# Performance work log

Measured on AMD Instinct MI355X. Metric: run time of the kernel, lower is better.

## Reference

```python
import jax, jax.numpy as jnp
import numpy as np

B, L, DM, H, PD = 2, 1024, 512, 8, 64
D = DM // H  # head_dim = 64
NEG = -10000.0


def setup_inputs() -> dict:
    key = jax.random.key(0)
    ks = jax.random.split(key, 12)
    s = 1.0 / np.sqrt(DM)
    sp = 1.0 / np.sqrt(PD)
    return {
        "x": jax.random.normal(ks[0], (B, L, DM), dtype=jnp.float32),
        "z": jax.random.normal(ks[1], (B, L, L, PD), dtype=jnp.float32),
        "residue_mask": jnp.ones((B, L), dtype=bool),
        "Wq": jax.random.normal(ks[2], (DM, DM), dtype=jnp.float32) * s,
        "bq": jnp.zeros((DM,), dtype=jnp.float32),
        "Wk": jax.random.normal(ks[3], (DM, DM), dtype=jnp.float32) * s,
        "bk": jnp.zeros((DM,), dtype=jnp.float32),
        "Wv": jax.random.normal(ks[4], (DM, DM), dtype=jnp.float32) * s,
        "bv": jnp.zeros((DM,), dtype=jnp.float32),
        "Wo": jax.random.normal(ks[5], (DM, DM), dtype=jnp.float32) * s,
        "bo": jnp.zeros((DM,), dtype=jnp.float32),
        "Wpb": jax.random.normal(ks[6], (PD, H), dtype=jnp.float32) * sp,
    }


def reference(x, z, residue_mask, Wq, bq, Wk, bk, Wv, bv, Wo, bo, Wpb):
    b, l, c = x.shape
    scale = 1.0 / np.sqrt(D)
    # projections -> (B, H, L, D)
    q = (x @ Wq + bq).reshape(b, l, H, D).transpose(0, 2, 1, 3)
    k = (x @ Wk + bk).reshape(b, l, H, D).transpose(0, 2, 1, 3)
    v = (x @ Wv + bv).reshape(b, l, H, D).transpose(0, 2, 1, 3)
    # pair bias: (B, L, L, PD) @ (PD, H) -> (B, H, L, L)
    bias = jnp.einsum('bijp,ph->bhij', z, Wpb)
    logits = jnp.einsum('bhid,bhjd->bhij', q, k) * scale + bias
    key_ok = residue_mask[:, None, None, :]
    query_ok = residue_mask[:, None, :, None]
    logits = jnp.where(key_ok, logits, NEG)
    logits = jnp.where(query_ok, logits, NEG)
    attn = jax.nn.softmax(logits, axis=-1)
    out = jnp.einsum('bhij,bhjd->bhid', attn, v)
    out = out.transpose(0, 2, 1, 3).reshape(b, l, c)
    return out @ Wo + bo
```

## Files before the change

### kernel.cpp

```cpp
#include <hip/hip_runtime.h>

typedef __bf16 bf16;
typedef __attribute__((ext_vector_type(4))) __bf16 bf16x4;
typedef __attribute__((ext_vector_type(8))) __bf16 bf16x8;
typedef __attribute__((ext_vector_type(4))) float f32x4;
typedef __attribute__((ext_vector_type(4))) _Float16 f16x4;
typedef __attribute__((ext_vector_type(2))) _Float16 f16x2;

#define B_   2
#define L_   1024
#define DM_  512
#define H_   8
#define D_   64
#define PD_  64
#define NEG_VAL -10000.0f

#define XB_N   (2048*512)
#define WT_N   (1536*512)
#define WTO_N  (512*512)
#define WTPB_N (16*64)

static __device__ __forceinline__ f32x4 mfma_bf16(bf16x8 a, bf16x8 b, f32x4 c) {
  return __builtin_amdgcn_mfma_f32_16x16x32_bf16(a, b, c, 0, 0, 0);
}

__global__ __launch_bounds__(256) void prep_kernel(
    const float* __restrict__ x, const float* __restrict__ Wq, const float* __restrict__ Wk,
    const float* __restrict__ Wv, const float* __restrict__ Wo, const float* __restrict__ Wpb,
    bf16* __restrict__ xb, bf16* __restrict__ Wt, bf16* __restrict__ Wto, bf16* __restrict__ Wtpb) {
  const int total = XB_N + WT_N + WTO_N + WTPB_N;
  for (int idx = blockIdx.x * 256 + threadIdx.x; idx < total; idx += gridDim.x * 256) {
    if (idx < XB_N) {
      xb[idx] = (bf16)x[idx];
    } else if (idx < XB_N + WT_N) {
      int t = idx - XB_N;
      int n = t >> 9, kk = t & 511;
      int sel = n >> 9, nn = n & 511;
      const float* W = sel == 0 ? Wq : (sel == 1 ? Wk : Wv);
      Wt[t] = (bf16)W[kk * 512 + nn];
    } else if (idx < XB_N + WT_N + WTO_N) {
      int t = idx - XB_N - WT_N;
      int n = t >> 9, kk = t & 511;
      Wto[t] = (bf16)Wo[kk * 512 + n];
    } else {
      int t = idx - XB_N - WT_N - WTO_N;
      int n = t >> 6, kk = t & 63;
      Wtpb[t] = (n < 8) ? (bf16)Wpb[kk * 8 + n] : (bf16)0.0f;
    }
  }
}

__global__ __launch_bounds__(256) void qkv_gemm(
    const bf16* __restrict__ xb, const bf16* __restrict__ Wt,
    const float* __restrict__ bq, const float* __restrict__ bk, const float* __restrict__ bv,
    bf16* __restrict__ qb, bf16* __restrict__ kb, bf16* __restrict__ vT) {
  int wid = blockIdx.x * 4 + (threadIdx.x >> 6);
  int lane = threadIdx.x & 63;
  int mt = wid / 48, nt = wid - mt * 48;
  int row0 = mt * 32, col0 = nt * 32;
  int lr = lane & 15, lg = lane >> 4;
  const bf16* a0p = xb + (row0 + lr) * 512 + lg * 8;
  const bf16* a1p = a0p + 16 * 512;
  const bf16* b0p = Wt + (col0 + lr) * 512 + lg * 8;
  const bf16* b1p = b0p + 16 * 512;
  f32x4 acc00 = {0.f,0.f,0.f,0.f}, acc01 = acc00, acc10 = acc00, acc11 = acc00;
#pragma unroll
  for (int kk = 0; kk < 512; kk += 32) {
    bf16x8 a0 = *reinterpret_cast<const bf16x8*>(a0p + kk);
    bf16x8 a1 = *reinterpret_cast<const bf16x8*>(a1p + kk);
    bf16x8 b0 = *reinterpret_cast<const bf16x8*>(b0p + kk);
    bf16x8 b1 = *reinterpret_cast<const bf16x8*>(b1p + kk);
    acc00 = mfma_bf16(a0, b0, acc00);
    acc01 = mfma_bf16(a0, b1, acc01);
    acc10 = mfma_bf16(a1, b0, acc10);
    acc11 = mfma_bf16(a1, b1, acc11);
  }
#pragma unroll
  for (int ni = 0; ni < 2; ++ni) {
    int col = col0 + ni * 16 + lr;
    int wsel = col >> 9;
    int ncol = col & 511;
    int h = ncol >> 6, d = ncol & 63;
    const float* bias = wsel == 0 ? bq : (wsel == 1 ? bk : bv);
    float bval = bias[ncol];
#pragma unroll
    for (int mi = 0; mi < 2; ++mi) {
      f32x4 acc = (mi == 0) ? (ni == 0 ? acc00 : acc01) : (ni == 0 ? acc10 : acc11);
      int m0 = row0 + mi * 16 + lg * 4;
      int bidx = m0 >> 10, l0 = m0 & 1023;
      if (wsel == 2) {
        bf16x4 pv;
#pragma unroll
        for (int r = 0; r < 4; ++r) pv[r] = (bf16)(acc[r] + bval);
        *reinterpret_cast<bf16x4*>(vT + ((long)(bidx * H_ + h) * D_ + d) * L_ + l0) = pv;
      } else if (wsel == 0) {
#pragma unroll
        for (int r = 0; r < 4; ++r)
          qb[((long)(bidx * H_ + h) * L_ + l0 + r) * D_ + d] = (bf16)((acc[r] + bval) * 0.125f);
      } else {
#pragma unroll
        for (int r = 0; r < 4; ++r)
          kb[((long)(bidx * H_ + h) * L_ + l0 + r) * D_ + d] = (bf16)(acc[r] + bval);
      }
    }
  }
}

__global__ __launch_bounds__(256) void fused_attn(
    const float* __restrict__ z, const bf16* __restrict__ qb, const bf16* __restrict__ kb,
    const bf16* __restrict__ vT, const bf16* __restrict__ Wtpb, const int* __restrict__ mask,
    _Float16* __restrict__ part_o, float* __restrict__ part_m, float* __restrict__ part_l) {
  __shared__ _Float16 bias_lds[8 * 16 * 64];
  __shared__ bf16 p_lds[4][16 * 64];
  int bid = blockIdx.x;
  int jc = bid & 15, it = (bid >> 4) & 63, b = bid >> 10;
  int i0 = it * 16, j0 = jc * 64;
  int tid = threadIdx.x, w = tid >> 6, lane = tid & 63, lr = lane & 15, lg = lane >> 4;

  bf16x8 wb0 = *reinterpret_cast<const bf16x8*>(Wtpb + lr * 64 + lg * 8);
  bf16x8 wb1 = *reinterpret_cast<const bf16x8*>(Wtpb + lr * 64 + 32 + lg * 8);

  {
    char* bl = (char*)bias_lds;
#pragma unroll
    for (int ii = 0; ii < 4; ++ii) {
      int i = w * 4 + ii;
      const float* zb_ = z + ((long)(b * L_ + i0 + i) * L_ + j0) * 64;
#pragma unroll
      for (int js = 0; js < 4; ++js) {
        const float* zr = zb_ + (js * 16 + lr) * 64 + lg * 8;
        f32x4 f0 = *reinterpret_cast<const f32x4*>(zr);
        f32x4 f1 = *reinterpret_cast<const f32x4*>(zr + 4);
        f32x4 f2 = *reinterpret_cast<const f32x4*>(zr + 32);
        f32x4 f3 = *reinterpret_cast<const f32x4*>(zr + 36);
        bf16x8 a0, a1;
#pragma unroll
        for (int e = 0; e < 4; ++e) {
          a0[e] = (bf16)f0[e]; a0[e + 4] = (bf16)f1[e];
          a1[e] = (bf16)f2[e]; a1[e + 4] = (bf16)f3[e];
        }
        f32x4 c = {0.f, 0.f, 0.f, 0.f};
        c = mfma_bf16(a0, wb0, c);
        c = mfma_bf16(a1, wb1, c);
        if (lr < 8) {
          f16x4 hv;
#pragma unroll
          for (int r = 0; r < 4; ++r) hv[r] = (_Float16)c[r];
          int X = (js * 32 + lg * 8) ^ ((i & 7) << 4) ^ ((lr & 3) << 5);
          *reinterpret_cast<f16x4*>(bl + lr * 2048 + i * 128 + X) = hv;
        }
      }
    }
  }
  __syncthreads();

  bool qok = mask[b * L_ + i0 + lr] != 0;
  char* pbuf = (char*)&p_lds[w][0];
  int swz = (lr & 7) << 4;
  const char* bl = (const char*)bias_lds;

#pragma unroll
  for (int hh = 0; hh < 2; ++hh) {
    int h = w * 2 + hh;
    const bf16* qrow = qb + ((long)(b * H_ + h) * L_ + i0 + lr) * D_ + lg * 8;
    bf16x8 qa0 = *reinterpret_cast<const bf16x8*>(qrow);
    bf16x8 qa1 = *reinterpret_cast<const bf16x8*>(qrow + 32);
    const bf16* kbase = kb + (long)(b * H_ + h) * L_ * D_;
    const bf16* vbase = vT + (long)(b * H_ + h) * D_ * L_;

    f32x4 s0, s1, s2, s3;
#pragma unroll
    for (int tile = 0; tile < 4; ++tile) {
      int X = (tile * 32 + lg * 8) ^ ((lr & 7) << 4) ^ ((h & 3) << 5);
      f16x4 bv = *reinterpret_cast<const f16x4*>(bl + h * 2048 + lr * 128 + X);
      f32x4 acc;
#pragma unroll
      for (int r = 0; r < 4; ++r) acc[r] = (float)bv[r];
      const bf16* kr = kbase + (long)(j0 + tile * 16 + lr) * D_ + lg * 8;
      acc = mfma_bf16(*reinterpret_cast<const bf16x8*>(kr), qa0, acc);
      acc = mfma_bf16(*reinterpret_cast<const bf16x8*>(kr + 32), qa1, acc);
      int4 mk = *reinterpret_cast<const int4*>(mask + b * L_ + j0 + tile * 16 + lg * 4);
      if (mk.x == 0) acc[0] = NEG_VAL;
      if (mk.y == 0) acc[1] = NEG_VAL;
      if (mk.z == 0) acc[2] = NEG_VAL;
      if (mk.w == 0) acc[3] = NEG_VAL;
      if (tile == 0) s0 = acc; else if (tile == 1) s1 = acc; else if (tile == 2) s2 = acc; else s3 = acc;
    }
    if (!qok) {
#pragma unroll
      for (int r = 0; r < 4; ++r) { s0[r] = NEG_VAL; s1[r] = NEG_VAL; s2[r] = NEG_VAL; s3[r] = NEG_VAL; }
    }
    float m = s0[0];
#pragma unroll
    for (int r = 0; r < 4; ++r) m = fmaxf(fmaxf(fmaxf(m, s0[r]), fmaxf(s1[r], s2[r])), s3[r]);
    m = fmaxf(m, __shfl_xor(m, 16));
    m = fmaxf(m, __shfl_xor(m, 32));
    f32x4 p0, p1, p2, p3;
    float ps = 0.f;
#pragma unroll
    for (int r = 0; r < 4; ++r) {
      p0[r] = __expf(s0[r] - m); p1[r] = __expf(s1[r] - m);
      p2[r] = __expf(s2[r] - m); p3[r] = __expf(s3[r] - m);
      ps += p0[r] + p1[r] + p2[r] + p3[r];
    }
    ps += __shfl_xor(ps, 16);
    ps += __shfl_xor(ps, 32);
#pragma unroll
    for (int tile = 0; tile < 4; ++tile) {
      f32x4 pv = (tile == 0) ? p0 : (tile == 1) ? p1 : (tile == 2) ? p2 : p3;
      bf16x4 pb_;
#pragma unroll
      for (int r = 0; r < 4; ++r) pb_[r] = (bf16)pv[r];
      *reinterpret_cast<bf16x4*>(pbuf + ((lr * 128 + tile * 32 + lg * 8) ^ swz)) = pb_;
    }
    bf16x8 pa0 = *reinterpret_cast<const bf16x8*>(pbuf + ((lr * 128 + lg * 16) ^ swz));
    bf16x8 pa1 = *reinterpret_cast<const bf16x8*>(pbuf + ((lr * 128 + 64 + lg * 16) ^ swz));
    long obase = ((long)bid * H_ + h) * 16;
#pragma unroll
    for (int dtile = 0; dtile < 4; ++dtile) {
      const bf16* vr = vbase + (long)(dtile * 16 + lr) * L_ + j0 + lg * 8;
      f32x4 acc = {0.f, 0.f, 0.f, 0.f};
      acc = mfma_bf16(*reinterpret_cast<const bf16x8*>(vr), pa0, acc);
      acc = mfma_bf16(*reinterpret_cast<const bf16x8*>(vr + 32), pa1, acc);
      f16x4 ov;
#pragma unroll
      for (int r = 0; r < 4; ++r) ov[r] = (_Float16)acc[r];
      *reinterpret_cast<f16x4*>(part_o + (obase + lr) * 64 + dtile * 16 + lg * 4) = ov;
    }
    if (lg == 0) { part_m[obase + lr] = m; part_l[obase + lr] = ps; }
  }
}

__global__ __launch_bounds__(256) void merge16(
    const _Float16* __restrict__ part_o, const float* __restrict__ part_m,
    const float* __restrict__ part_l, bf16* __restrict__ attn_out) {
  int t = blockIdx.x * 256 + threadIdx.x;
  int d0 = (t & 15) * 4;
  int row = t >> 4;
  int b = row >> 13, h = (row >> 10) & 7, i = row & 1023;
  int it = i >> 4, il = i & 15;
  int bid0 = (b << 10) + (it << 4);
  float mv[16];
  float M = -3.0e38f;
#pragma unroll
  for (int p = 0; p < 16; ++p) {
    long base = ((long)(bid0 + p) * H_ + h) * 16 + il;
    mv[p] = part_m[base];
    M = fmaxf(M, mv[p]);
  }
  float lt = 0.f;
  float oa[4] = {0.f, 0.f, 0.f, 0.f};
#pragma unroll
  for (int p = 0; p < 16; ++p) {
    long base = ((long)(bid0 + p) * H_ + h) * 16 + il;
    float c = __expf(mv[p] - M);
    lt += c * part_l[base];
    f16x4 ov = *reinterpret_cast<const f16x4*>(part_o + base * 64 + d0);
#pragma unroll
    for (int e = 0; e < 4; ++e) oa[e] += c * (float)ov[e];
  }
  float inv = 1.0f / lt;
  bf16x4 r_;
#pragma unroll
  for (int e = 0; e < 4; ++e) r_[e] = (bf16)(oa[e] * inv);
  *reinterpret_cast<bf16x4*>(attn_out + ((long)(b * L_ + i)) * DM_ + h * D_ + d0) = r_;
}

__global__ __launch_bounds__(256) void out_gemm(
    const bf16* __restrict__ ab, const bf16* __restrict__ Wto,
    const float* __restrict__ bo, float* __restrict__ out) {
  int wid = blockIdx.x * 4 + (threadIdx.x >> 6);
  int lane = threadIdx.x & 63;
  int mt = wid >> 4, nt = wid & 15;
  int row0 = mt * 32, col0 = nt * 32;
  int lr = lane & 15, lg = lane >> 4;
  const bf16* a0p = ab + (row0 + lr) * 512 + lg * 8;
  const bf16* a1p = a0p + 16 * 512;
  const bf16* b0p = Wto + (col0 + lr) * 512 + lg * 8;
  const bf16* b1p = b0p + 16 * 512;
  f32x4 acc00 = {0.f,0.f,0.f,0.f}, acc01 = acc00, acc10 = acc00, acc11 = acc00;
#pragma unroll
  for (int kk = 0; kk < 512; kk += 32) {
    bf16x8 a0 = *reinterpret_cast<const bf16x8*>(a0p + kk);
    bf16x8 a1 = *reinterpret_cast<const bf16x8*>(a1p + kk);
    bf16x8 b0 = *reinterpret_cast<const bf16x8*>(b0p + kk);
    bf16x8 b1 = *reinterpret_cast<const bf16x8*>(b1p + kk);
    acc00 = mfma_bf16(a0, b0, acc00);
    acc01 = mfma_bf16(a0, b1, acc01);
    acc10 = mfma_bf16(a1, b0, acc10);
    acc11 = mfma_bf16(a1, b1, acc11);
  }
#pragma unroll
  for (int ni = 0; ni < 2; ++ni) {
    int col = col0 + ni * 16 + lr;
    float bval = bo[col];
#pragma unroll
    for (int mi = 0; mi < 2; ++mi) {
      f32x4 acc = (mi == 0) ? (ni == 0 ? acc00 : acc01) : (ni == 0 ? acc10 : acc11);
      int m0 = row0 + mi * 16 + lg * 4;
#pragma unroll
      for (int r = 0; r < 4; ++r) out[(long)(m0 + r) * 512 + col] = acc[r] + bval;
    }
  }
}

extern "C" void kernel_launch(void* const* d_in, const int* in_sizes, int n_in,
                              void* d_out, int out_size, void* d_ws, size_t ws_size,
                              hipStream_t stream) {
  const float* x    = (const float*)d_in[0];
  const float* z    = (const float*)d_in[1];
  const int*   mask = (const int*)d_in[2];
  const float* Wq   = (const float*)d_in[3];
  const float* bq   = (const float*)d_in[4];
  const float* Wk   = (const float*)d_in[5];
  const float* bk   = (const float*)d_in[6];
  const float* Wv   = (const float*)d_in[7];
  const float* bv   = (const float*)d_in[8];
  const float* Wo   = (const float*)d_in[9];
  const float* bo   = (const float*)d_in[10];
  const float* Wpb  = (const float*)d_in[11];

  char* ws = (char*)d_ws;
  bf16* xb        = (bf16*)(ws + 0);
  bf16* Wt        = (bf16*)(ws + 2097152);
  bf16* Wto       = (bf16*)(ws + 3670016);
  bf16* Wtpb      = (bf16*)(ws + 4194304);
  bf16* qbuf      = (bf16*)(ws + 4196352);
  bf16* kbuf      = (bf16*)(ws + 6293504);
  bf16* vTbuf     = (bf16*)(ws + 8390656);
  bf16* attn_out  = (bf16*)(ws + 10487808);
  _Float16* part_o = (_Float16*)(ws + 12584960);
  float* part_m   = (float*)(ws + 46139392);
  float* part_l   = (float*)(ws + 47187968);

  prep_kernel<<<2048, 256, 0, stream>>>(x, Wq, Wk, Wv, Wo, Wpb, xb, Wt, Wto, Wtpb);
  qkv_gemm<<<768, 256, 0, stream>>>(xb, Wt, bq, bk, bv, qbuf, kbuf, vTbuf);
  fused_attn<<<2048, 256, 0, stream>>>(z, qbuf, kbuf, vTbuf, Wtpb, mask, part_o, part_m, part_l);
  merge16<<<1024, 256, 0, stream>>>(part_o, part_m, part_l, attn_out);
  out_gemm<<<256, 256, 0, stream>>>(attn_out, Wto, bo, (float*)d_out);
}
```

Measured before the change: 188.5 us.

## Warp-specialize fused attention with double-buffered pair-bias producer warps

```diff
diff --git a/kernel.cpp b/kernel.cpp
--- a/kernel.cpp
+++ b/kernel.cpp
@@ -106,128 +106,176 @@
   }
 }
 
-__global__ __launch_bounds__(256) void fused_attn(
+__global__ __launch_bounds__(512) void fused_attn(
     const float* __restrict__ z, const bf16* __restrict__ qb, const bf16* __restrict__ kb,
     const bf16* __restrict__ vT, const bf16* __restrict__ Wtpb, const int* __restrict__ mask,
     _Float16* __restrict__ part_o, float* __restrict__ part_m, float* __restrict__ part_l) {
-  __shared__ _Float16 bias_lds[8 * 16 * 64];
+  __shared__ _Float16 bias_lds[2][8 * 16 * 64];
   __shared__ bf16 p_lds[4][16 * 64];
   int bid = blockIdx.x;
-  int jc = bid & 15, it = (bid >> 4) & 63, b = bid >> 10;
-  int i0 = it * 16, j0 = jc * 64;
+  int jg = bid & 3, it = (bid >> 2) & 63, b = bid >> 8;
+  int i0 = it * 16;
   int tid = threadIdx.x, w = tid >> 6, lane = tid & 63, lr = lane & 15, lg = lane >> 4;
-
-  bf16x8 wb0 = *reinterpret_cast<const bf16x8*>(Wtpb + lr * 64 + lg * 8);
-  bf16x8 wb1 = *reinterpret_cast<const bf16x8*>(Wtpb + lr * 64 + 32 + lg * 8);
-
-  {
-    char* bl = (char*)bias_lds;
-#pragma unroll
-    for (int ii = 0; ii < 4; ++ii) {
-      int i = w * 4 + ii;
-      const float* zb_ = z + ((long)(b * L_ + i0 + i) * L_ + j0) * 64;
-#pragma unroll
-      for (int js = 0; js < 4; ++js) {
-        const float* zr = zb_ + (js * 16 + lr) * 64 + lg * 8;
-        f32x4 f0 = *reinterpret_cast<const f32x4*>(zr);
-        f32x4 f1 = *reinterpret_cast<const f32x4*>(zr + 4);
-        f32x4 f2 = *reinterpret_cast<const f32x4*>(zr + 32);
-        f32x4 f3 = *reinterpret_cast<const f32x4*>(zr + 36);
-        bf16x8 a0, a1;
-#pragma unroll
-        for (int e = 0; e < 4; ++e) {
-          a0[e] = (bf16)f0[e]; a0[e + 4] = (bf16)f1[e];
-          a1[e] = (bf16)f2[e]; a1[e + 4] = (bf16)f3[e];
-        }
-        f32x4 c = {0.f, 0.f, 0.f, 0.f};
-        c = mfma_bf16(a0, wb0, c);
-        c = mfma_bf16(a1, wb1, c);
-        if (lr < 8) {
-          f16x4 hv;
-#pragma unroll
-          for (int r = 0; r < 4; ++r) hv[r] = (_Float16)c[r];
-          int X = (js * 32 + lg * 8) ^ ((i & 7) << 4) ^ ((lr & 3) << 5);
-          *reinterpret_cast<f16x4*>(bl + lr * 2048 + i * 128 + X) = hv;
+  bool producer = w < 4;
+
+  if (producer) {
+    int pw = w;
+    bf16x8 wb0 = *reinterpret_cast<const bf16x8*>(Wtpb + lr * 64 + lg * 8);
+    bf16x8 wb1 = *reinterpret_cast<const bf16x8*>(Wtpb + lr * 64 + 32 + lg * 8);
+    {
+      char* bl = (char*)&bias_lds[0][0];
+      int j0 = jg * 256;
+#pragma unroll
+      for (int ii = 0; ii < 4; ++ii) {
+        int i = pw * 4 + ii;
+        const float* zb_ = z + ((long)(b * L_ + i0 + i) * L_ + j0) * 64;
+#pragma unroll
+        for (int js = 0; js < 4; ++js) {
+          const float* zr = zb_ + (js * 16 + lr) * 64 + lg * 8;
+          f32x4 f0 = *reinterpret_cast<const f32x4*>(zr);
+          f32x4 f1 = *reinterpret_cast<const f32x4*>(zr + 4);
+          f32x4 f2 = *reinterpret_cast<const f32x4*>(zr + 32);
+          f32x4 f3 = *reinterpret_cast<const f32x4*>(zr + 36);
+          bf16x8 a0, a1;
+#pragma unroll
+          for (int e = 0; e < 4; ++e) {
+            a0[e] = (bf16)f0[e]; a0[e + 4] = (bf16)f1[e];
+            a1[e] = (bf16)f2[e]; a1[e + 4] = (bf16)f3[e];
+          }
+          f32x4 c = {0.f, 0.f, 0.f, 0.f};
+          c = mfma_bf16(a0, wb0, c);
+          c = mfma_bf16(a1, wb1, c);
+          if (lr < 8) {
+            f16x4 hv;
+#pragma unroll
+            for (int r = 0; r < 4; ++r) hv[r] = (_Float16)c[r];
+            int X = (js * 32 + lg * 8) ^ ((i & 7) << 4) ^ ((lr & 3) << 5);
+            *reinterpret_cast<f16x4*>(bl + lr * 2048 + i * 128 + X) = hv;
+          }
         }
       }
     }
-  }
-  __syncthreads();
-
-  bool qok = mask[b * L_ + i0 + lr] != 0;
-  char* pbuf = (char*)&p_lds[w][0];
-  int swz = (lr & 7) << 4;
-  const char* bl = (const char*)bias_lds;
-
-#pragma unroll
-  for (int hh = 0; hh < 2; ++hh) {
-    int h = w * 2 + hh;
-    const bf16* qrow = qb + ((long)(b * H_ + h) * L_ + i0 + lr) * D_ + lg * 8;
-    bf16x8 qa0 = *reinterpret_cast<const bf16x8*>(qrow);
-    bf16x8 qa1 = *reinterpret_cast<const bf16x8*>(qrow + 32);
-    const bf16* kbase = kb + (long)(b * H_ + h) * L_ * D_;
-    const bf16* vbase = vT + (long)(b * H_ + h) * D_ * L_;
-
-    f32x4 s0, s1, s2, s3;
-#pragma unroll
-    for (int tile = 0; tile < 4; ++tile) {
-      int X = (tile * 32 + lg * 8) ^ ((lr & 7) << 4) ^ ((h & 3) << 5);
-      f16x4 bv = *reinterpret_cast<const f16x4*>(bl + h * 2048 + lr * 128 + X);
-      f32x4 acc;
-#pragma unroll
-      for (int r = 0; r < 4; ++r) acc[r] = (float)bv[r];
-      const bf16* kr = kbase + (long)(j0 + tile * 16 + lr) * D_ + lg * 8;
-      acc = mfma_bf16(*reinterpret_cast<const bf16x8*>(kr), qa0, acc);
-      acc = mfma_bf16(*reinterpret_cast<const bf16x8*>(kr + 32), qa1, acc);
-      int4 mk = *reinterpret_cast<const int4*>(mask + b * L_ + j0 + tile * 16 + lg * 4);
-      if (mk.x == 0) acc[0] = NEG_VAL;
-      if (mk.y == 0) acc[1] = NEG_VAL;
-      if (mk.z == 0) acc[2] = NEG_VAL;
-      if (mk.w == 0) acc[3] = NEG_VAL;
-      if (tile == 0) s0 = acc; else if (tile == 1) s1 = acc; else if (tile == 2) s2 = acc; else s3 = acc;
-    }
-    if (!qok) {
-#pragma unroll
-      for (int r = 0; r < 4; ++r) { s0[r] = NEG_VAL; s1[r] = NEG_VAL; s2[r] = NEG_VAL; s3[r] = NEG_VAL; }
-    }
-    float m = s0[0];
-#pragma unroll
-    for (int r = 0; r < 4; ++r) m = fmaxf(fmaxf(fmaxf(m, s0[r]), fmaxf(s1[r], s2[r])), s3[r]);
-    m = fmaxf(m, __shfl_xor(m, 16));
-    m = fmaxf(m, __shfl_xor(m, 32));
-    f32x4 p0, p1, p2, p3;
-    float ps = 0.f;
-#pragma unroll
-    for (int r = 0; r < 4; ++r) {
-      p0[r] = __expf(s0[r] - m); p1[r] = __expf(s1[r] - m);
-      p2[r] = __expf(s2[r] - m); p3[r] = __expf(s3[r] - m);
-      ps += p0[r] + p1[r] + p2[r] + p3[r];
-    }
-    ps += __shfl_xor(ps, 16);
-    ps += __shfl_xor(ps, 32);
-#pragma unroll
-    for (int tile = 0; tile < 4; ++tile) {
-      f32x4 pv = (tile == 0) ? p0 : (tile == 1) ? p1 : (tile == 2) ? p2 : p3;
-      bf16x4 pb_;
-#pragma unroll
-      for (int r = 0; r < 4; ++r) pb_[r] = (bf16)pv[r];
-      *reinterpret_cast<bf16x4*>(pbuf + ((lr * 128 + tile * 32 + lg * 8) ^ swz)) = pb_;
-    }
-    bf16x8 pa0 = *reinterpret_cast<const bf16x8*>(pbuf + ((lr * 128 + lg * 16) ^ swz));
-    bf16x8 pa1 = *reinterpret_cast<const bf16x8*>(pbuf + ((lr * 128 + 64 + lg * 16) ^ swz));
-    long obase = ((long)bid * H_ + h) * 16;
-#pragma unroll
-    for (int dtile = 0; dtile < 4; ++dtile) {
-      const bf16* vr = vbase + (long)(dtile * 16 + lr) * L_ + j0 + lg * 8;
-      f32x4 acc = {0.f, 0.f, 0.f, 0.f};
-      acc = mfma_bf16(*reinterpret_cast<const bf16x8*>(vr), pa0, acc);
-      acc = mfma_bf16(*reinterpret_cast<const bf16x8*>(vr + 32), pa1, acc);
-      f16x4 ov;
-#pragma unroll
-      for (int r = 0; r < 4; ++r) ov[r] = (_Float16)acc[r];
-      *reinterpret_cast<f16x4*>(part_o + (obase + lr) * 64 + dtile * 16 + lg * 4) = ov;
-    }
-    if (lg == 0) { part_m[obase + lr] = m; part_l[obase + lr] = ps; }
+    for (int t = 0; t < 4; ++t) {
+      __syncthreads();
+      if (t < 3) {
+        char* bl = (char*)&bias_lds[(t + 1) & 1][0];
+        int j0 = (jg * 4 + t + 1) * 64;
+#pragma unroll
+        for (int ii = 0; ii < 4; ++ii) {
+          int i = pw * 4 + ii;
+          const float* zb_ = z + ((long)(b * L_ + i0 + i) * L_ + j0) * 64;
+#pragma unroll
+          for (int js = 0; js < 4; ++js) {
+            const float* zr = zb_ + (js * 16 + lr) * 64 + lg * 8;
+            f32x4 f0 = *reinterpret_cast<const f32x4*>(zr);
+            f32x4 f1 = *reinterpret_cast<const f32x4*>(zr + 4);
+            f32x4 f2 = *reinterpret_cast<const f32x4*>(zr + 32);
+            f32x4 f3 = *reinterpret_cast<const f32x4*>(zr + 36);
+            bf16x8 a0, a1;
+#pragma unroll
+            for (int e = 0; e < 4; ++e) {
+              a0[e] = (bf16)f0[e]; a0[e + 4] = (bf16)f1[e];
+              a1[e] = (bf16)f2[e]; a1[e + 4] = (bf16)f3[e];
+            }
+            f32x4 c = {0.f, 0.f, 0.f, 0.f};
+            c = mfma_bf16(a0, wb0, c);
+            c = mfma_bf16(a1, wb1, c);
+            if (lr < 8) {
+              f16x4 hv;
+#pragma unroll
+              for (int r = 0; r < 4; ++r) hv[r] = (_Float16)c[r];
+              int X = (js * 32 + lg * 8) ^ ((i & 7) << 4) ^ ((lr & 3) << 5);
+              *reinterpret_cast<f16x4*>(bl + lr * 2048 + i * 128 + X) = hv;
+            }
+          }
+        }
+      }
+    }
+  } else {
+    int cw = w - 4;
+    bool qok = mask[b * L_ + i0 + lr] != 0;
+    char* pbuf = (char*)&p_lds[cw][0];
+    int swz = (lr & 7) << 4;
+    const bf16* qrow0 = qb + ((long)(b * H_ + cw * 2) * L_ + i0 + lr) * D_ + lg * 8;
+    const bf16* qrow1 = qb + ((long)(b * H_ + cw * 2 + 1) * L_ + i0 + lr) * D_ + lg * 8;
+    bf16x8 qa00 = *reinterpret_cast<const bf16x8*>(qrow0);
+    bf16x8 qa01 = *reinterpret_cast<const bf16x8*>(qrow0 + 32);
+    bf16x8 qa10 = *reinterpret_cast<const bf16x8*>(qrow1);
+    bf16x8 qa11 = *reinterpret_cast<const bf16x8*>(qrow1 + 32);
+    for (int t = 0; t < 4; ++t) {
+      __syncthreads();
+      int j0 = (jg * 4 + t) * 64;
+      long cid = ((long)(b * 64 + it) << 4) + jg * 4 + t;
+      const char* bl = (const char*)&bias_lds[t & 1][0];
+#pragma unroll
+      for (int hh = 0; hh < 2; ++hh) {
+        int h = cw * 2 + hh;
+        bf16x8 qa0 = hh == 0 ? qa00 : qa10;
+        bf16x8 qa1 = hh == 0 ? qa01 : qa11;
+        const bf16* kbase = kb + (long)(b * H_ + h) * L_ * D_;
+        const bf16* vbase = vT + (long)(b * H_ + h) * D_ * L_;
+        f32x4 s0, s1, s2, s3;
+#pragma unroll
+        for (int tile = 0; tile < 4; ++tile) {
+          int X = (tile * 32 + lg * 8) ^ ((lr & 7) << 4) ^ ((h & 3) << 5);
+          f16x4 bv = *reinterpret_cast<const f16x4*>(bl + h * 2048 + lr * 128 + X);
+          f32x4 acc;
+#pragma unroll
+          for (int r = 0; r < 4; ++r) acc[r] = (float)bv[r];
+          const bf16* kr = kbase + (long)(j0 + tile * 16 + lr) * D_ + lg * 8;
+          acc = mfma_bf16(*reinterpret_cast<const bf16x8*>(kr), qa0, acc);
+          acc = mfma_bf16(*reinterpret_cast<const bf16x8*>(kr + 32), qa1, acc);
+          int4 mk = *reinterpret_cast<const int4*>(mask + b * L_ + j0 + tile * 16 + lg * 4);
+          if (mk.x == 0) acc[0] = NEG_VAL;
+          if (mk.y == 0) acc[1] = NEG_VAL;
+          if (mk.z == 0) acc[2] = NEG_VAL;
+          if (mk.w == 0) acc[3] = NEG_VAL;
+          if (tile == 0) s0 = acc; else if (tile == 1) s1 = acc; else if (tile == 2) s2 = acc; else s3 = acc;
+        }
+        if (!qok) {
+#pragma unroll
+          for (int r = 0; r < 4; ++r) { s0[r] = NEG_VAL; s1[r] = NEG_VAL; s2[r] = NEG_VAL; s3[r] = NEG_VAL; }
+        }
+        float m = s0[0];
+#pragma unroll
+        for (int r = 0; r < 4; ++r) m = fmaxf(fmaxf(fmaxf(m, s0[r]), fmaxf(s1[r], s2[r])), s3[r]);
+        m = fmaxf(m, __shfl_xor(m, 16));
+        m = fmaxf(m, __shfl_xor(m, 32));
+        f32x4 p0, p1, p2, p3;
+        float ps = 0.f;
+#pragma unroll
+        for (int r = 0; r < 4; ++r) {
+          p0[r] = __expf(s0[r] - m); p1[r] = __expf(s1[r] - m);
+          p2[r] = __expf(s2[r] - m); p3[r] = __expf(s3[r] - m);
+          ps += p0[r] + p1[r] + p2[r] + p3[r];
+        }
+        ps += __shfl_xor(ps, 16);
+        ps += __shfl_xor(ps, 32);
+#pragma unroll
+        for (int tile = 0; tile < 4; ++tile) {
+          f32x4 pv = (tile == 0) ? p0 : (tile == 1) ? p1 : (tile == 2) ? p2 : p3;
+          bf16x4 pb_;
+#pragma unroll
+          for (int r = 0; r < 4; ++r) pb_[r] = (bf16)pv[r];
+          *reinterpret_cast<bf16x4*>(pbuf + ((lr * 128 + tile * 32 + lg * 8) ^ swz)) = pb_;
+        }
+        bf16x8 pa0 = *reinterpret_cast<const bf16x8*>(pbuf + ((lr * 128 + lg * 16) ^ swz));
+        bf16x8 pa1 = *reinterpret_cast<const bf16x8*>(pbuf + ((lr * 128 + 64 + lg * 16) ^ swz));
+        long obase = (cid * H_ + h) * 16;
+#pragma unroll
+        for (int dtile = 0; dtile < 4; ++dtile) {
+          const bf16* vr = vbase + (long)(dtile * 16 + lr) * L_ + j0 + lg * 8;
+          f32x4 acc = {0.f, 0.f, 0.f, 0.f};
+          acc = mfma_bf16(*reinterpret_cast<const bf16x8*>(vr), pa0, acc);
+          acc = mfma_bf16(*reinterpret_cast<const bf16x8*>(vr + 32), pa1, acc);
+          f16x4 ov;
+#pragma unroll
+          for (int r = 0; r < 4; ++r) ov[r] = (_Float16)acc[r];
+          *reinterpret_cast<f16x4*>(part_o + (obase + lr) * 64 + dtile * 16 + lg * 4) = ov;
+        }
+        if (lg == 0) { part_m[obase + lr] = m; part_l[obase + lr] = ps; }
+      }
+    }
   }
 }
 
@@ -335,7 +383,7 @@
 
   prep_kernel<<<2048, 256, 0, stream>>>(x, Wq, Wk, Wv, Wo, Wpb, xb, Wt, Wto, Wtpb);
   qkv_gemm<<<768, 256, 0, stream>>>(xb, Wt, bq, bk, bv, qbuf, kbuf, vTbuf);
-  fused_attn<<<2048, 256, 0, stream>>>(z, qbuf, kbuf, vTbuf, Wtpb, mask, part_o, part_m, part_l);
+  fused_attn<<<512, 512, 0, stream>>>(z, qbuf, kbuf, vTbuf, Wtpb, mask, part_o, part_m, part_l);
   merge16<<<1024, 256, 0, stream>>>(part_o, part_m, part_l, attn_out);
   out_gemm<<<256, 256, 0, stream>>>(attn_out, Wto, bo, (float*)d_out);
 }
```

After: 187.4 us. About the same (-0.6%).

## Warp-specialize fused attention into z-bias producers and attention consumers

Applied to the files above, without the earlier changes.

```diff
diff --git a/kernel.cpp b/kernel.cpp
--- a/kernel.cpp
+++ b/kernel.cpp
@@ -19,6 +19,8 @@
 #define WT_N   (1536*512)
 #define WTO_N  (512*512)
 #define WTPB_N (16*64)
+
+#define NPROD 6
 
 static __device__ __forceinline__ f32x4 mfma_bf16(bf16x8 a, bf16x8 b, f32x4 c) {
   return __builtin_amdgcn_mfma_f32_16x16x32_bf16(a, b, c, 0, 0, 0);
@@ -106,128 +108,135 @@
   }
 }
 
-__global__ __launch_bounds__(256) void fused_attn(
+static __device__ __forceinline__ void produce_chunk(
+    const float* __restrict__ z, char* bl, int b, int i0, int j0,
+    int pw, int lr, int lg, bf16x8 wb0, bf16x8 wb1) {
+  for (int u = pw; u < 64; u += NPROD) {
+    int i = u >> 2, js = u & 3;
+    const float* zr = z + ((long)(b * L_ + i0 + i) * L_ + j0 + js * 16 + lr) * 64 + lg * 8;
+    f32x4 f0 = *reinterpret_cast<const f32x4*>(zr);
+    f32x4 f1 = *reinterpret_cast<const f32x4*>(zr + 4);
+    f32x4 f2 = *reinterpret_cast<const f32x4*>(zr + 32);
+    f32x4 f3 = *reinterpret_cast<const f32x4*>(zr + 36);
+    bf16x8 a0, a1;
+#pragma unroll
+    for (int e = 0; e < 4; ++e) {
+      a0[e] = (bf16)f0[e]; a0[e + 4] = (bf16)f1[e];
+      a1[e] = (bf16)f2[e]; a1[e + 4] = (bf16)f3[e];
+    }
+    f32x4 c = {0.f, 0.f, 0.f, 0.f};
+    c = mfma_bf16(a0, wb0, c);
+    c = mfma_bf16(a1, wb1, c);
+    if (lr < 8) {
+      f16x4 hv;
+#pragma unroll
+      for (int r = 0; r < 4; ++r) hv[r] = (_Float16)c[r];
+      int X = (js * 32 + lg * 8) ^ ((i & 7) << 4) ^ ((lr & 3) << 5);
+      *reinterpret_cast<f16x4*>(bl + lr * 2048 + i * 128 + X) = hv;
+    }
+  }
+}
+
+__global__ __launch_bounds__(512, 8) void fused_attn(
     const float* __restrict__ z, const bf16* __restrict__ qb, const bf16* __restrict__ kb,
     const bf16* __restrict__ vT, const bf16* __restrict__ Wtpb, const int* __restrict__ mask,
     _Float16* __restrict__ part_o, float* __restrict__ part_m, float* __restrict__ part_l) {
-  __shared__ _Float16 bias_lds[8 * 16 * 64];
-  __shared__ bf16 p_lds[4][16 * 64];
+  __shared__ _Float16 bias_lds[2][8 * 16 * 64];
+  __shared__ bf16 p_lds[2][16 * 64];
   int bid = blockIdx.x;
-  int jc = bid & 15, it = (bid >> 4) & 63, b = bid >> 10;
-  int i0 = it * 16, j0 = jc * 64;
+  int jg = bid & 7, it = (bid >> 3) & 63, b = bid >> 9;
+  int i0 = it * 16;
   int tid = threadIdx.x, w = tid >> 6, lane = tid & 63, lr = lane & 15, lg = lane >> 4;
 
-  bf16x8 wb0 = *reinterpret_cast<const bf16x8*>(Wtpb + lr * 64 + lg * 8);
-  bf16x8 wb1 = *reinterpret_cast<const bf16x8*>(Wtpb + lr * 64 + 32 + lg * 8);
-
-  {
-    char* bl = (char*)bias_lds;
-#pragma unroll
-    for (int ii = 0; ii < 4; ++ii) {
-      int i = w * 4 + ii;
-      const float* zb_ = z + ((long)(b * L_ + i0 + i) * L_ + j0) * 64;
-#pragma unroll
-      for (int js = 0; js < 4; ++js) {
-        const float* zr = zb_ + (js * 16 + lr) * 64 + lg * 8;
-        f32x4 f0 = *reinterpret_cast<const f32x4*>(zr);
-        f32x4 f1 = *reinterpret_cast<const f32x4*>(zr + 4);
-        f32x4 f2 = *reinterpret_cast<const f32x4*>(zr + 32);
-        f32x4 f3 = *reinterpret_cast<const f32x4*>(zr + 36);
-        bf16x8 a0, a1;
-#pragma unroll
-        for (int e = 0; e < 4; ++e) {
-          a0[e] = (bf16)f0[e]; a0[e + 4] = (bf16)f1[e];
-          a1[e] = (bf16)f2[e]; a1[e + 4] = (bf16)f3[e];
-        }
-        f32x4 c = {0.f, 0.f, 0.f, 0.f};
-        c = mfma_bf16(a0, wb0, c);
-        c = mfma_bf16(a1, wb1, c);
-        if (lr < 8) {
-          f16x4 hv;
-#pragma unroll
-          for (int r = 0; r < 4; ++r) hv[r] = (_Float16)c[r];
-          int X = (js * 32 + lg * 8) ^ ((i & 7) << 4) ^ ((lr & 3) << 5);
-          *reinterpret_cast<f16x4*>(bl + lr * 2048 + i * 128 + X) = hv;
-        }
+  if (w < NPROD) {
+    bf16x8 wb0 = *reinterpret_cast<const bf16x8*>(Wtpb + lr * 64 + lg * 8);
+    bf16x8 wb1 = *reinterpret_cast<const bf16x8*>(Wtpb + lr * 64 + 32 + lg * 8);
+    produce_chunk(z, (char*)&bias_lds[0][0], b, i0, (jg * 2) * 64, w, lr, lg, wb0, wb1);
+    for (int t = 0; t < 2; ++t) {
+      __syncthreads();
+      if (t < 1)
+        produce_chunk(z, (char*)&bias_lds[1][0], b, i0, (jg * 2 + 1) * 64, w, lr, lg, wb0, wb1);
+    }
+  } else {
+    int cw = w - NPROD;
+    bool qok = mask[b * L_ + i0 + lr] != 0;
+    char* pbuf = (char*)&p_lds[cw][0];
+    int swz = (lr & 7) << 4;
+    for (int t = 0; t < 2; ++t) {
+      __syncthreads();
+      int j0 = (jg * 2 + t) * 64;
+      long cid = ((long)(b * 64 + it) << 4) + jg * 2 + t;
+      const char* bl = (const char*)&bias_lds[t & 1][0];
+#pragma unroll
+      for (int hh = 0; hh < 4; ++hh) {
+        int h = cw * 4 + hh;
+        const bf16* qrow = qb + ((long)(b * H_ + h) * L_ + i0 + lr) * D_ + lg * 8;
+        bf16x8 qa0 = *reinterpret_cast<const bf16x8*>(qrow);
+        bf16x8 qa1 = *reinterpret_cast<const bf16x8*>(qrow + 32);
+        const bf16* kbase = kb + (long)(b * H_ + h) * L_ * D_;
+        const bf16* vbase = vT + (long)(b * H_ + h) * D_ * L_;
+        f32x4 s0, s1, s2, s3;
+#pragma unroll
+        for (int tile = 0; tile < 4; ++tile) {
+          int X = (tile * 32 + lg * 8) ^ ((lr & 7) << 4) ^ ((h & 3) << 5);
+          f16x4 bv = *reinterpret_cast<const f16x4*>(bl + h * 2048 + lr * 128 + X);
+          f32x4 acc;
+#pragma unroll
+          for (int r = 0; r < 4; ++r) acc[r] = (float)bv[r];
+          const bf16* kr = kbase + (long)(j0 + tile * 16 + lr) * D_ + lg * 8;
+          acc = mfma_bf16(*reinterpret_cast<const bf16x8*>(kr), qa0, acc);
+          acc = mfma_bf16(*reinterpret_cast<const bf16x8*>(kr + 32), qa1, acc);
+          int4 mk = *reinterpret_cast<const int4*>(mask + b * L_ + j0 + tile * 16 + lg * 4);
+          if (mk.x == 0) acc[0] = NEG_VAL;
+          if (mk.y == 0) acc[1] = NEG_VAL;
+          if (mk.z == 0) acc[2] = NEG_VAL;
+          if (mk.w == 0) acc[3] = NEG_VAL;
+          if (tile == 0) s0 = acc; else if (tile == 1) s1 = acc; else if (tile == 2) s2 = acc; else s3 = acc;
+        }
+        if (!qok) {
+#pragma unroll
+          for (int r = 0; r < 4; ++r) { s0[r] = NEG_VAL; s1[r] = NEG_VAL; s2[r] = NEG_VAL; s3[r] = NEG_VAL; }
+        }
+        float m = s0[0];
+#pragma unroll
+        for (int r = 0; r < 4; ++r) m = fmaxf(fmaxf(fmaxf(m, s0[r]), fmaxf(s1[r], s2[r])), s3[r]);
+        m = fmaxf(m, __shfl_xor(m, 16));
+        m = fmaxf(m, __shfl_xor(m, 32));
+        f32x4 p0, p1, p2, p3;
+        float ps = 0.f;
+#pragma unroll
+        for (int r = 0; r < 4; ++r) {
+          p0[r] = __expf(s0[r] - m); p1[r] = __expf(s1[r] - m);
+          p2[r] = __expf(s2[r] - m); p3[r] = __expf(s3[r] - m);
+          ps += p0[r] + p1[r] + p2[r] + p3[r];
+        }
+        ps += __shfl_xor(ps, 16);
+        ps += __shfl_xor(ps, 32);
+#pragma unroll
+        for (int tile = 0; tile < 4; ++tile) {
+          f32x4 pv = (tile == 0) ? p0 : (tile == 1) ? p1 : (tile == 2) ? p2 : p3;
+          bf16x4 pb_;
+#pragma unroll
+          for (int r = 0; r < 4; ++r) pb_[r] = (bf16)pv[r];
+          *reinterpret_cast<bf16x4*>(pbuf + ((lr * 128 + tile * 32 + lg * 8) ^ swz)) = pb_;
+        }
+        bf16x8 pa0 = *reinterpret_cast<const bf16x8*>(pbuf + ((lr * 128 + lg * 16) ^ swz));
+        bf16x8 pa1 = *reinterpret_cast<const bf16x8*>(pbuf + ((lr * 128 + 64 + lg * 16) ^ swz));
+        long obase = (cid * H_ + h) * 16;
+#pragma unroll
+        for (int dtile = 0; dtile < 4; ++dtile) {
+          const bf16* vr = vbase + (long)(dtile * 16 + lr) * L_ + j0 + lg * 8;
+          f32x4 acc = {0.f, 0.f, 0.f, 0.f};
+          acc = mfma_bf16(*reinterpret_cast<const bf16x8*>(vr), pa0, acc);
+          acc = mfma_bf16(*reinterpret_cast<const bf16x8*>(vr + 32), pa1, acc);
+          f16x4 ov;
+#pragma unroll
+          for (int r = 0; r < 4; ++r) ov[r] = (_Float16)acc[r];
+          *reinterpret_cast<f16x4*>(part_o + (obase + lr) * 64 + dtile * 16 + lg * 4) = ov;
+        }
+        if (lg == 0) { part_m[obase + lr] = m; part_l[obase + lr] = ps; }
       }
     }
-  }
-  __syncthreads();
-
-  bool qok = mask[b * L_ + i0 + lr] != 0;
-  char* pbuf = (char*)&p_lds[w][0];
-  int swz = (lr & 7) << 4;
-  const char* bl = (const char*)bias_lds;
-
-#pragma unroll
-  for (int hh = 0; hh < 2; ++hh) {
-    int h = w * 2 + hh;
-    const bf16* qrow = qb + ((long)(b * H_ + h) * L_ + i0 + lr) * D_ + lg * 8;
-    bf16x8 qa0 = *reinterpret_cast<const bf16x8*>(qrow);
-    bf16x8 qa1 = *reinterpret_cast<const bf16x8*>(qrow + 32);
-    const bf16* kbase = kb + (long)(b * H_ + h) * L_ * D_;
-    const bf16* vbase = vT + (long)(b * H_ + h) * D_ * L_;
-
-    f32x4 s0, s1, s2, s3;
-#pragma unroll
-    for (int tile = 0; tile < 4; ++tile) {
-      int X = (tile * 32 + lg * 8) ^ ((lr & 7) << 4) ^ ((h & 3) << 5);
-      f16x4 bv = *reinterpret_cast<const f16x4*>(bl + h * 2048 + lr * 128 + X);
-      f32x4 acc;
-#pragma unroll
-      for (int r = 0; r < 4; ++r) acc[r] = (float)bv[r];
-      const bf16* kr = kbase + (long)(j0 + tile * 16 + lr) * D_ + lg * 8;
-      acc = mfma_bf16(*reinterpret_cast<const bf16x8*>(kr), qa0, acc);
-      acc = mfma_bf16(*reinterpret_cast<const bf16x8*>(kr + 32), qa1, acc);
-      int4 mk = *reinterpret_cast<const int4*>(mask + b * L_ + j0 + tile * 16 + lg * 4);
-      if (mk.x == 0) acc[0] = NEG_VAL;
-      if (mk.y == 0) acc[1] = NEG_VAL;
-      if (mk.z == 0) acc[2] = NEG_VAL;
-      if (mk.w == 0) acc[3] = NEG_VAL;
-      if (tile == 0) s0 = acc; else if (tile == 1) s1 = acc; else if (tile == 2) s2 = acc; else s3 = acc;
-    }
-    if (!qok) {
-#pragma unroll
-      for (int r = 0; r < 4; ++r) { s0[r] = NEG_VAL; s1[r] = NEG_VAL; s2[r] = NEG_VAL; s3[r] = NEG_VAL; }
-    }
-    float m = s0[0];
-#pragma unroll
-    for (int r = 0; r < 4; ++r) m = fmaxf(fmaxf(fmaxf(m, s0[r]), fmaxf(s1[r], s2[r])), s3[r]);
-    m = fmaxf(m, __shfl_xor(m, 16));
-    m = fmaxf(m, __shfl_xor(m, 32));
-    f32x4 p0, p1, p2, p3;
-    float ps = 0.f;
-#pragma unroll
-    for (int r = 0; r < 4; ++r) {
-      p0[r] = __expf(s0[r] - m); p1[r] = __expf(s1[r] - m);
-      p2[r] = __expf(s2[r] - m); p3[r] = __expf(s3[r] - m);
-      ps += p0[r] + p1[r] + p2[r] + p3[r];
-    }
-    ps += __shfl_xor(ps, 16);
-    ps += __shfl_xor(ps, 32);
-#pragma unroll
-    for (int tile = 0; tile < 4; ++tile) {
-      f32x4 pv = (tile == 0) ? p0 : (tile == 1) ? p1 : (tile == 2) ? p2 : p3;
-      bf16x4 pb_;
-#pragma unroll
-      for (int r = 0; r < 4; ++r) pb_[r] = (bf16)pv[r];
-      *reinterpret_cast<bf16x4*>(pbuf + ((lr * 128 + tile * 32 + lg * 8) ^ swz)) = pb_;
-    }
-    bf16x8 pa0 = *reinterpret_cast<const bf16x8*>(pbuf + ((lr * 128 + lg * 16) ^ swz));
-    bf16x8 pa1 = *reinterpret_cast<const bf16x8*>(pbuf + ((lr * 128 + 64 + lg * 16) ^ swz));
-    long obase = ((long)bid * H_ + h) * 16;
-#pragma unroll
-    for (int dtile = 0; dtile < 4; ++dtile) {
-      const bf16* vr = vbase + (long)(dtile * 16 + lr) * L_ + j0 + lg * 8;
-      f32x4 acc = {0.f, 0.f, 0.f, 0.f};
-      acc = mfma_bf16(*reinterpret_cast<const bf16x8*>(vr), pa0, acc);
-      acc = mfma_bf16(*reinterpret_cast<const bf16x8*>(vr + 32), pa1, acc);
-      f16x4 ov;
-#pragma unroll
-      for (int r = 0; r < 4; ++r) ov[r] = (_Float16)acc[r];
-      *reinterpret_cast<f16x4*>(part_o + (obase + lr) * 64 + dtile * 16 + lg * 4) = ov;
-    }
-    if (lg == 0) { part_m[obase + lr] = m; part_l[obase + lr] = ps; }
   }
 }
 
@@ -335,7 +344,7 @@
 
   prep_kernel<<<2048, 256, 0, stream>>>(x, Wq, Wk, Wv, Wo, Wpb, xb, Wt, Wto, Wtpb);
   qkv_gemm<<<768, 256, 0, stream>>>(xb, Wt, bq, bk, bv, qbuf, kbuf, vTbuf);
-  fused_attn<<<2048, 256, 0, stream>>>(z, qbuf, kbuf, vTbuf, Wtpb, mask, part_o, part_m, part_l);
+  fused_attn<<<1024, 512, 0, stream>>>(z, qbuf, kbuf, vTbuf, Wtpb, mask, part_o, part_m, part_l);
   merge16<<<1024, 256, 0, stream>>>(part_o, part_m, part_l, attn_out);
   out_gemm<<<256, 256, 0, stream>>>(attn_out, Wto, bo, (float*)d_out);
 }
```

Result: slower. 243.2 us (+29.0%).
